# Optimization experiments

Measured on AMD Instinct MI355X. Metric: run time of the kernel, lower is better.

Reference implementation:

```python
import jax, jax.numpy as jnp
import numpy as np

N = 50000        # num nodes
E = 500000       # num edges
F_IN = 128       # in_channels
F_OUT = 128      # out_channels
C = 2            # num_channels
E_DIM = 64       # edge_dim
NEG = 0.2        # leaky_relu negative slope


def setup_inputs() -> dict:
    key = jax.random.key(0)
    ks = jax.random.split(key, 8)
    glorot = lambda k, s: jax.random.normal(k, s, jnp.float32) * (1.0 / np.float32(np.sqrt(s[-1])))
    return {
        "x": jax.random.normal(ks[0], (N, F_IN), jnp.float32),
        "edge_index": jax.random.randint(ks[1], (2, E), 0, N, dtype=jnp.int32),
        "edge_attr": jax.random.normal(ks[2], (E, E_DIM), jnp.float32),
        "W_l": glorot(ks[3], (F_OUT, F_IN)),
        "channel_bias_l": jnp.zeros((C, F_OUT), jnp.float32),
        "att_shared": glorot(ks[4], (F_OUT,)),
        "att_scale": glorot(ks[5], (C,)),
        "W_edge": glorot(ks[6], (F_OUT, E_DIM)),
        "edge_bias": jnp.zeros((F_OUT, C), jnp.float32),
    }


def reference(x, edge_index, edge_attr, W_l, channel_bias_l, att_shared, att_scale, W_edge, edge_bias):
    src, tgt = edge_index[0], edge_index[1]
    # shared projection (share_weights=True -> x_r has no channel bias)
    x_base = x @ W_l.T                                      # [N, F]
    x_l = x_base[:, :, None] + channel_bias_l.T[None]       # [N, F, C]
    x_i = x_l[tgt]                                          # [E, F, C] gather targets
    x_j = x_base[src]                                       # [E, F]    gather sources (same for all channels)
    # edge embedding expanded over channels + per-channel edge bias
    edge_emb = (edge_attr @ W_edge.T)[:, :, None] + edge_bias[None]   # [E, F, C]
    attn = jax.nn.leaky_relu(x_i + x_j[:, :, None] + edge_emb, NEG)   # [E, F, C]
    # per-channel attention logits
    logits = jnp.einsum('efc,f->ec', attn, att_shared) * att_scale[None, :]  # [E, C]
    # segment softmax over target nodes (numerically stable)
    m = jax.ops.segment_max(logits, tgt, num_segments=N)    # [N, C]
    m = jnp.where(jnp.isfinite(m), m, 0.0)
    e = jnp.exp(logits - m[tgt])
    s = jax.ops.segment_sum(e, tgt, num_segments=N)
    alpha = e / (s[tgt] + 1e-16)                            # [E, C]
    # weighted messages and scatter-add aggregation
    msgs = (x_j[:, :, None] + edge_emb) * alpha[:, None, :] # [E, F, C]
    agg = jax.ops.segment_sum(msgs, tgt, num_segments=N)    # [N, F, C]
    # concat=True: channel-major concat along feature dim -> [N, C*F]
    out = agg.transpose(0, 2, 1).reshape(N, C * F_OUT)
    return out, alpha
```

## Files before the change

### kernel.cpp

```cpp
#include <hip/hip_runtime.h>
#include <hip/hip_bf16.h>

#define NN 50000
#define NE 500000
#define F 128
#define K_IN 128
#define ED 64
#define C 2
#define NEG 0.2f
#define FLTMAX 3.402823466e38f
#define PROJ_BLOCKS 782
#define HIST_BLOCKS 1954

typedef __attribute__((ext_vector_type(8))) short short8;
typedef __attribute__((ext_vector_type(8))) unsigned short ushort8;
typedef __attribute__((ext_vector_type(4))) float f32x4;

__device__ __forceinline__ short bf16r(float f) {
    unsigned u = __float_as_uint(f);
    unsigned r = (u + 0x7fffu + ((u >> 16) & 1u)) >> 16;
    return (short)r;
}

__device__ __forceinline__ float b2f(unsigned short v) {
    return __uint_as_float(((unsigned)v) << 16);
}

__device__ __forceinline__ short8 ldfrag(const float* base) {
    const float4* p = reinterpret_cast<const float4*>(base);
    float4 v0 = p[0], v1 = p[1];
    short8 r;
    r[0] = bf16r(v0.x); r[1] = bf16r(v0.y); r[2] = bf16r(v0.z); r[3] = bf16r(v0.w);
    r[4] = bf16r(v1.x); r[5] = bf16r(v1.y); r[6] = bf16r(v1.z); r[7] = bf16r(v1.w);
    return r;
}

__device__ __forceinline__ short8 cvt8(float4 v0, float4 v1) {
    short8 r;
    r[0] = bf16r(v0.x); r[1] = bf16r(v0.y); r[2] = bf16r(v0.z); r[3] = bf16r(v0.w);
    r[4] = bf16r(v1.x); r[5] = bf16r(v1.y); r[6] = bf16r(v1.z); r[7] = bf16r(v1.w);
    return r;
}

__global__ __launch_bounds__(256) void proj_hist(const float* __restrict__ x,
                                                 const float* __restrict__ W_l,
                                                 unsigned short* __restrict__ xbp,
                                                 const int* __restrict__ ei,
                                                 int* __restrict__ counts) {
    if (blockIdx.x < PROJ_BLOCKS) {
        int lane = threadIdx.x & 63, wid = threadIdx.x >> 6;
        int grp = lane >> 4, col = lane & 15;
        int tile = blockIdx.x * 4 + wid;
        if (tile >= NN / 16) return;
        int n0 = tile * 16;

        f32x4 acc[8];
#pragma unroll
        for (int t = 0; t < 8; ++t) acc[t] = (f32x4){0.f, 0.f, 0.f, 0.f};

        const float* arow = x + (size_t)(n0 + col) * K_IN + grp * 8;
#pragma unroll
        for (int kt = 0; kt < 4; ++kt) {
            short8 a = ldfrag(arow + kt * 32);
#pragma unroll
            for (int t = 0; t < 8; ++t) {
                short8 b = ldfrag(W_l + (size_t)(t * 16 + col) * K_IN + kt * 32 + grp * 8);
                acc[t] = __builtin_amdgcn_mfma_f32_16x16x32_bf16(a, b, acc[t], 0, 0, 0);
            }
        }
#pragma unroll
        for (int j = 0; j < 4; ++j) {
            ushort8 o;
#pragma unroll
            for (int t = 0; t < 8; ++t) o[t] = (unsigned short)bf16r(acc[t][j]);
            *reinterpret_cast<ushort8*>(xbp + (size_t)(n0 + grp * 4 + j) * F + col * 8) = o;
        }
    } else {
        int e = (blockIdx.x - PROJ_BLOCKS) * 256 + threadIdx.x;
        if (e < NE) atomicAdd(&counts[ei[NE + e]], 1);
    }
}

__global__ __launch_bounds__(1024) void scan1_kernel(const int* __restrict__ counts,
                                                     int* __restrict__ offs,
                                                     int* __restrict__ bsum) {
    __shared__ int wsum[16];
    int i = blockIdx.x * 1024 + threadIdx.x;
    int lane = threadIdx.x & 63, w = threadIdx.x >> 6;
    int v = (i < NN) ? counts[i] : 0;
    int x = v;
#pragma unroll
    for (int off = 1; off < 64; off <<= 1) {
        int y = __shfl_up(x, off, 64);
        if (lane >= off) x += y;
    }
    if (lane == 63) wsum[w] = x;
    __syncthreads();
    if (w == 0 && lane < 16) {
        int t = wsum[lane];
#pragma unroll
        for (int off = 1; off < 16; off <<= 1) {
            int y = __shfl_up(t, off, 16);
            if (lane >= off) t += y;
        }
        wsum[lane] = t;
    }
    __syncthreads();
    int woff = (w == 0) ? 0 : wsum[w - 1];
    if (i < NN) offs[i] = woff + x - v;
    if (threadIdx.x == 1023) bsum[blockIdx.x] = woff + x;
}

__global__ __launch_bounds__(1024) void scan3b_kernel(int* __restrict__ offs,
                                                      const int* __restrict__ bsum,
                                                      int* __restrict__ cursor) {
    __shared__ int carry_s;
    if (threadIdx.x < 64) {
        int v = (threadIdx.x < blockIdx.x) ? bsum[threadIdx.x] : 0;
#pragma unroll
        for (int off = 32; off; off >>= 1) v += __shfl_xor(v, off, 64);
        if (threadIdx.x == 0) carry_s = v;
    }
    __syncthreads();
    int carry = carry_s;
    int i = blockIdx.x * 1024 + threadIdx.x;
    if (i < NN) {
        int o = offs[i] + carry;
        offs[i] = o;
        cursor[i] = o;
    }
    if (blockIdx.x == 0 && threadIdx.x == 0) offs[NN] = NE;
}

__global__ void scatter_kernel(const int* __restrict__ ei, int* __restrict__ cursor,
                               int2* __restrict__ perm2, int* __restrict__ tgts) {
    int e = blockIdx.x * blockDim.x + threadIdx.x;
    if (e < NE) {
        int src = ei[e];
        int tgt = ei[NE + e];
        int p = atomicAdd(&cursor[tgt], 1);
        int2 v; v.x = e; v.y = src;
        perm2[p] = v;
        tgts[p] = tgt;
    }
}

template<int MODE>
__global__ __launch_bounds__(256) void edge_logits_mfma(
    const int2* __restrict__ perm2, const int* __restrict__ tgts,
    const float* __restrict__ ea,
    const unsigned short* __restrict__ xbp, const float* __restrict__ W_e,
    const float* __restrict__ cb, const float* __restrict__ att,
    const float* __restrict__ att_sc, const float* __restrict__ ebias,
    float* __restrict__ lgs, unsigned short* __restrict__ msg) {
    int lane = threadIdx.x & 63, wid = threadIdx.x >> 6;
    int grp = lane >> 4, col = lane & 15;

    short8 B[8][2];
#pragma unroll
    for (int t = 0; t < 8; ++t)
#pragma unroll
        for (int kt = 0; kt < 2; ++kt)
            B[t][kt] = ldfrag(W_e + (size_t)(t * 16 + col) * ED + kt * 32 + grp * 8);

    float attv[8], cbe0[8], cbe1[8];
#pragma unroll
    for (int t = 0; t < 8; ++t) {
        int f = t * 16 + col;
        attv[t] = att[f];
        cbe0[t] = cb[f] + ebias[f * 2];
        cbe1[t] = cb[F + f] + ebias[f * 2 + 1];
    }
    float as0 = att_sc[0], as1 = att_sc[1];
    float2* lgs2 = reinterpret_cast<float2*>(lgs);

    const int NT = NE / 16;
    const int stride = gridDim.x * 4;
    int tile = blockIdx.x * 4 + wid;

    int2 pe = {0, 0};
    int tgtv = 0;
    float4 rc0, rc1, rc2, rc3;
    if (tile < NT) {
        pe = perm2[tile * 16 + col];
        tgtv = tgts[tile * 16 + col];
        const float* base = ea + (size_t)pe.x * ED + grp * 8;
        const float4* ap = reinterpret_cast<const float4*>(base);
        rc0 = ap[0]; rc1 = ap[1];
        const float4* ap2 = reinterpret_cast<const float4*>(base + 32);
        rc2 = ap2[0]; rc3 = ap2[1];
    }

    for (; tile < NT; tile += stride) {
        int tn = tile + stride;
        int2 pe_n = {0, 0};
        int tgt_n = 0;
        float4 rn0 = {}, rn1 = {}, rn2 = {}, rn3 = {};
        if (tn < NT) {
            pe_n = perm2[tn * 16 + col];
            tgt_n = tgts[tn * 16 + col];
            const float* base = ea + (size_t)pe_n.x * ED + grp * 8;
            const float4* ap = reinterpret_cast<const float4*>(base);
            rn0 = ap[0]; rn1 = ap[1];
            const float4* ap2 = reinterpret_cast<const float4*>(base + 32);
            rn2 = ap2[0]; rn3 = ap2[1];
        }

        int p0 = tile * 16;
        int srcv = pe.y;
        int tgti[4];
        ushort8 xsv[4];
#pragma unroll
        for (int j = 0; j < 4; ++j) {
            int idx = grp * 4 + j;
            int src = __shfl(srcv, idx, 16);
            tgti[j] = __shfl(tgtv, idx, 16);
            xsv[j] = *reinterpret_cast<const ushort8*>(
                xbp + (size_t)src * F + col * 8);
        }

        short8 a0 = cvt8(rc0, rc1);
        short8 a1 = cvt8(rc2, rc3);
        f32x4 acc[8];
#pragma unroll
        for (int t = 0; t < 8; ++t) acc[t] = (f32x4){0.f, 0.f, 0.f, 0.f};
#pragma unroll
        for (int t = 0; t < 8; ++t) {
            acc[t] = __builtin_amdgcn_mfma_f32_16x16x32_bf16(a0, B[t][0], acc[t], 0, 0, 0);
            acc[t] = __builtin_amdgcn_mfma_f32_16x16x32_bf16(a1, B[t][1], acc[t], 0, 0, 0);
        }
#pragma unroll
        for (int j = 0; j < 4; ++j) {
            int idx = grp * 4 + j;
            ushort8 xs = xsv[j];
            ushort8 xt = *reinterpret_cast<const ushort8*>(
                xbp + (size_t)tgti[j] * F + col * 8);
            float q0 = 0.f, q1 = 0.f;
            ushort8 mvs;
#pragma unroll
            for (int t = 0; t < 8; ++t) {
                float mv = b2f(xs[t]) + acc[t][j];
                mvs[t] = (unsigned short)bf16r(mv);
                float s = mv + b2f(xt[t]);
                float u0 = s + cbe0[t]; u0 = fmaxf(u0, NEG * u0);
                float u1 = s + cbe1[t]; u1 = fmaxf(u1, NEG * u1);
                q0 = fmaf(u0, attv[t], q0);
                q1 = fmaf(u1, attv[t], q1);
            }
            if (MODE >= 1)
                *reinterpret_cast<ushort8*>(msg + (size_t)(p0 + idx) * F + col * 8) = mvs;
#pragma unroll
            for (int off = 8; off; off >>= 1) {
                q0 += __shfl_xor(q0, off, 16);
                q1 += __shfl_xor(q1, off, 16);
            }
            if (col == 0) {
                float2 o; o.x = q0 * as0; o.y = q1 * as1;
                lgs2[p0 + idx] = o;
            }
        }
        pe = pe_n; tgtv = tgt_n;
        rc0 = rn0; rc1 = rn1; rc2 = rn2; rc3 = rn3;
    }
}

__global__ __launch_bounds__(512) void agg_msg(
    const int* __restrict__ offs, const int2* __restrict__ perm2,
    const unsigned short* __restrict__ msg, const float* __restrict__ ebias,
    const float* __restrict__ lgs,
    float* __restrict__ out, float* __restrict__ alpha_out) {
    int lane = threadIdx.x & 63;
    int node = blockIdx.x * 8 + (threadIdx.x >> 6);
    if (node >= NN) return;
    int beg = offs[node], end = offs[node + 1];
    int deg = end - beg;
    float* orow = out + (size_t)node * (C * F);
    float2* orow2 = reinterpret_cast<float2*>(orow);
    if (deg == 0) {
        float2 z; z.x = 0.f; z.y = 0.f;
        orow2[lane] = z; orow2[64 + lane] = z;
        return;
    }
    const float2* lgs2 = reinterpret_cast<const float2*>(lgs);
    float2* al2 = reinterpret_cast<float2*>(alpha_out);

    float m0 = -FLTMAX, m1 = -FLTMAX;
    for (int j = beg + lane; j < end; j += 64) {
        float2 lg = lgs2[j];
        m0 = fmaxf(m0, lg.x); m1 = fmaxf(m1, lg.y);
    }
#pragma unroll
    for (int off = 32; off; off >>= 1) {
        m0 = fmaxf(m0, __shfl_xor(m0, off, 64));
        m1 = fmaxf(m1, __shfl_xor(m1, off, 64));
    }
    float su0 = 0.f, su1 = 0.f;
    for (int j = beg + lane; j < end; j += 64) {
        float2 lg = lgs2[j];
        su0 += __expf(lg.x - m0); su1 += __expf(lg.y - m1);
    }
#pragma unroll
    for (int off = 32; off; off >>= 1) {
        su0 += __shfl_xor(su0, off, 64);
        su1 += __shfl_xor(su1, off, 64);
    }
    float inv0 = 1.f / (su0 + 1e-16f), inv1 = 1.f / (su1 + 1e-16f);

    float g00 = 0.f, g01 = 0.f, g10 = 0.f, g11 = 0.f;
    for (int cb0 = beg; cb0 < end; cb0 += 64) {
        int cnt = min(64, end - cb0);
        int jl = cb0 + min(lane, cnt - 1);
        bool act = lane < cnt;
        int el = perm2[jl].x;
        float2 lgl = lgs2[jl];
        float e0v = act ? __expf(lgl.x - m0) : 0.f;
        float e1v = act ? __expf(lgl.y - m1) : 0.f;
        if (act) { float2 av; av.x = e0v * inv0; av.y = e1v * inv1; al2[el] = av; }
#pragma unroll 4
        for (int i = 0; i < cnt; ++i) {
            float a0 = __shfl(e0v, i, 64) * inv0;
            float a1 = __shfl(e1v, i, 64) * inv1;
            unsigned mv = *reinterpret_cast<const unsigned*>(
                msg + (size_t)(cb0 + i) * F + lane * 2);
            float f0 = __uint_as_float((mv & 0xffffu) << 16);
            float f1 = __uint_as_float(mv & 0xffff0000u);
            g00 = fmaf(a0, f0, g00); g01 = fmaf(a0, f1, g01);
            g10 = fmaf(a1, f0, g10); g11 = fmaf(a1, f1, g11);
        }
    }
    float sa0 = su0 * inv0, sa1 = su1 * inv1;
    int q0i = 2 * lane;
    int f0i = (q0i & 7) * 16 + (q0i >> 3);
    int f1i = f0i + 16;
    orow[f0i]       = g00 + ebias[f0i * 2] * sa0;
    orow[f1i]       = g01 + ebias[f1i * 2] * sa0;
    orow[F + f0i]   = g10 + ebias[f0i * 2 + 1] * sa1;
    orow[F + f1i]   = g11 + ebias[f1i * 2 + 1] * sa1;
}

__device__ __forceinline__ float xbval(const unsigned short* __restrict__ xbp,
                                       int n, int f) {
    return b2f(xbp[(size_t)n * F + (f & 15) * 8 + (f >> 4)]);
}

__global__ __launch_bounds__(512) void agg_fast(
    const int* __restrict__ offs, const int2* __restrict__ perm2,
    const float* __restrict__ ea, const unsigned short* __restrict__ xbp,
    const float* __restrict__ ebias, const float* __restrict__ lgs,
    float* __restrict__ out, float* __restrict__ alpha_out,
    float* __restrict__ H) {
    int lane = threadIdx.x & 63;
    int node = blockIdx.x * 8 + (threadIdx.x >> 6);
    if (node >= NN) return;
    int beg = offs[node], end = offs[node + 1];
    int deg = end - beg;
    float* orow = out + (size_t)node * (C * F);
    float* hrow = H + (size_t)node * (C * ED);

    if (deg == 0) {
        orow[lane] = 0.f; orow[64 + lane] = 0.f;
        orow[128 + lane] = 0.f; orow[192 + lane] = 0.f;
        if (lane < 32) { hrow[lane * 4] = 0.f; hrow[lane * 4 + 1] = 0.f;
                         hrow[lane * 4 + 2] = 0.f; hrow[lane * 4 + 3] = 0.f; }
        return;
    }
    const float2* lgs2 = reinterpret_cast<const float2*>(lgs);
    float2* al2 = reinterpret_cast<float2*>(alpha_out);

    float m0 = -FLTMAX, m1 = -FLTMAX;
    for (int j = beg + lane; j < end; j += 64) {
        float2 lg = lgs2[j];
        m0 = fmaxf(m0, lg.x); m1 = fmaxf(m1, lg.y);
    }
#pragma unroll
    for (int off = 32; off; off >>= 1) {
        m0 = fmaxf(m0, __shfl_xor(m0, off, 64));
        m1 = fmaxf(m1, __shfl_xor(m1, off, 64));
    }
    float s0 = 0.f, s1 = 0.f;
    for (int j = beg + lane; j < end; j += 64) {
        float2 lg = lgs2[j];
        s0 += __expf(lg.x - m0); s1 += __expf(lg.y - m1);
    }
#pragma unroll
    for (int off = 32; off; off >>= 1) {
        s0 += __shfl_xor(s0, off, 64);
        s1 += __shfl_xor(s1, off, 64);
    }
    float inv0 = 1.f / (s0 + 1e-16f), inv1 = 1.f / (s1 + 1e-16f);

    float h0 = 0.f, h1 = 0.f;
    float g00 = 0.f, g01 = 0.f, g10 = 0.f, g11 = 0.f;
    for (int j = beg; j < end; ++j) {
        int2 pe; pe.x = __builtin_amdgcn_readfirstlane(perm2[j].x);
        pe.y = __builtin_amdgcn_readfirstlane(perm2[j].y);
        float2 lg = lgs2[j];
        float a0 = __builtin_amdgcn_readfirstlane(__expf(lg.x - m0)) * inv0;
        float a1 = __builtin_amdgcn_readfirstlane(__expf(lg.y - m1)) * inv1;
        if (lane == 0) { float2 av; av.x = a0; av.y = a1; al2[pe.x] = av; }
        float av = ea[(size_t)pe.x * ED + lane];
        h0 = fmaf(a0, av, h0); h1 = fmaf(a1, av, h1);
        float xv0 = xbval(xbp, pe.y, lane);
        float xv1 = xbval(xbp, pe.y, 64 + lane);
        g00 = fmaf(a0, xv0, g00); g01 = fmaf(a1, xv0, g01);
        g10 = fmaf(a0, xv1, g10); g11 = fmaf(a1, xv1, g11);
    }
    hrow[lane] = h0; hrow[64 + lane] = h1;
    float sa0 = s0 * inv0, sa1 = s1 * inv1;
    orow[lane]       = g00 + ebias[lane * 2] * sa0;
    orow[64 + lane]  = g10 + ebias[(64 + lane) * 2] * sa0;
    orow[128 + lane] = g01 + ebias[lane * 2 + 1] * sa1;
    orow[192 + lane] = g11 + ebias[(64 + lane) * 2 + 1] * sa1;
}

__global__ __launch_bounds__(512) void emb_gemm(const float* __restrict__ H,
                                                const float* __restrict__ W_e,
                                                float* __restrict__ out) {
    __shared__ float WeT[ED][F];
    for (int i = threadIdx.x; i < ED * F; i += 512) {
        int f = i & (F - 1), k = i >> 7;
        WeT[k][f] = W_e[(size_t)f * ED + k];
    }
    __syncthreads();
    int lane = threadIdx.x & 63, wid = threadIdx.x >> 6;
    const int R = NN * C;
    for (int row = blockIdx.x * 8 + wid; row < R; row += gridDim.x * 8) {
        float h = H[(size_t)row * ED + lane];
        float m0 = 0.f, m1 = 0.f;
#pragma unroll
        for (int k = 0; k < ED; ++k) {
            float hk = __shfl(h, k, 64);
            m0 = fmaf(hk, WeT[k][lane], m0);
            m1 = fmaf(hk, WeT[k][lane + 64], m1);
        }
        float* op = out + (size_t)row * F;
        op[lane] += m0;
        op[lane + 64] += m1;
    }
}

extern "C" void kernel_launch(void* const* d_in, const int* in_sizes, int n_in,
                              void* d_out, int out_size, void* d_ws, size_t ws_size,
                              hipStream_t stream) {
    const float* x      = (const float*)d_in[0];
    const int*   ei     = (const int*)d_in[1];
    const float* ea     = (const float*)d_in[2];
    const float* W_l    = (const float*)d_in[3];
    const float* cb     = (const float*)d_in[4];
    const float* att    = (const float*)d_in[5];
    const float* att_sc = (const float*)d_in[6];
    const float* W_e    = (const float*)d_in[7];
    const float* ebias  = (const float*)d_in[8];

    float* out = (float*)d_out;
    float* alpha_out = out + (size_t)NN * C * F;

    float* ws = (float*)d_ws;
    unsigned short* xbp = (unsigned short*)ws;
    float* lgs  = ws + 6400000;
    int* ibase  = (int*)(ws + 7400000);
    int* counts = ibase;
    int* offs   = ibase + NN;
    int* bsum   = ibase + 100064;
    int* tgts   = ibase + 100128;
    int2* perm2 = (int2*)(ibase + 100128 + NE);
    char* tail = (char*)(ibase + 100128 + 3 * NE);
    tail = (char*)(((size_t)tail + 15) & ~(size_t)15);
    size_t head_bytes = (size_t)(tail - (char*)d_ws);
    size_t msg_bytes = (size_t)NE * F * 2;
    bool use_msg = ws_size >= head_bytes + msg_bytes + 64;
    unsigned short* msg = (unsigned short*)tail;
    float* H = (float*)tail;

    hipMemsetAsync(counts, 0, NN * sizeof(int), stream);

    proj_hist<<<PROJ_BLOCKS + HIST_BLOCKS, 256, 0, stream>>>(x, W_l, xbp, ei, counts);

    const int NB = (NN + 1023) / 1024;
    scan1_kernel<<<NB, 1024, 0, stream>>>(counts, offs, bsum);
    scan3b_kernel<<<NB, 1024, 0, stream>>>(offs, bsum, counts);
    scatter_kernel<<<(NE + 255) / 256, 256, 0, stream>>>(ei, counts, perm2, tgts);

    if (use_msg) {
        edge_logits_mfma<1><<<2048, 256, 0, stream>>>(perm2, tgts, ea, xbp, W_e,
                                                      cb, att, att_sc, ebias,
                                                      lgs, msg);
        agg_msg<<<(NN + 7) / 8, 512, 0, stream>>>(offs, perm2, msg, ebias, lgs,
                                                  out, alpha_out);
    } else {
        edge_logits_mfma<0><<<2048, 256, 0, stream>>>(perm2, tgts, ea, xbp, W_e,
                                                      cb, att, att_sc, ebias,
                                                      lgs, (unsigned short*)0);
        agg_fast<<<(NN + 7) / 8, 512, 0, stream>>>(offs, perm2, ea, xbp, ebias, lgs,
                                                   out, alpha_out, H);
        emb_gemm<<<1024, 512, 0, stream>>>(H, W_e, out);
    }
}
```

Before: 252.5 us.

## Stage edge-weight fragments in LDS and deepen gather prefetch in edge logits kernel

Moves the W_edge bf16 MFMA B-fragments from per-thread registers into shared memory to free registers. The index loads (perm2/tgts) are prefetched two tiles ahead instead of one, and the target-row gather is hoisted next to the source-row gather so both are in flight before the MFMAs. This aims to hide the latency of the dependent gathers and may raise occupancy. In exchange it adds LDS reads inside the hot loop, a block barrier at startup, and extra live registers for the deeper prefetch.

```diff
diff --git a/kernel.cpp b/kernel.cpp
--- a/kernel.cpp
+++ b/kernel.cpp
@@ -153,15 +153,15 @@
     const float* __restrict__ cb, const float* __restrict__ att,
     const float* __restrict__ att_sc, const float* __restrict__ ebias,
     float* __restrict__ lgs, unsigned short* __restrict__ msg) {
+    __shared__ short8 Blds[16][64];
     int lane = threadIdx.x & 63, wid = threadIdx.x >> 6;
     int grp = lane >> 4, col = lane & 15;
 
-    short8 B[8][2];
-#pragma unroll
-    for (int t = 0; t < 8; ++t)
-#pragma unroll
-        for (int kt = 0; kt < 2; ++kt)
-            B[t][kt] = ldfrag(W_e + (size_t)(t * 16 + col) * ED + kt * 32 + grp * 8);
+    for (int fidx = threadIdx.x; fidx < 1024; fidx += 256) {
+        int l = fidx & 63, kt = (fidx >> 6) & 1, t = fidx >> 7;
+        int g2 = l >> 4, c2 = l & 15;
+        Blds[t * 2 + kt][l] = ldfrag(W_e + (size_t)(t * 16 + c2) * ED + kt * 32 + g2 * 8);
+    }
 
     float attv[8], cbe0[8], cbe1[8];
 #pragma unroll
@@ -173,17 +173,27 @@
     }
     float as0 = att_sc[0], as1 = att_sc[1];
     float2* lgs2 = reinterpret_cast<float2*>(lgs);
+    __syncthreads();
 
     const int NT = NE / 16;
     const int stride = gridDim.x * 4;
     int tile = blockIdx.x * 4 + wid;
 
-    int2 pe = {0, 0};
-    int tgtv = 0;
+    int2 pe = {0, 0}, pe_n = {0, 0};
+    int tgtv = 0, tgt_n = 0;
     float4 rc0, rc1, rc2, rc3;
     if (tile < NT) {
         pe = perm2[tile * 16 + col];
         tgtv = tgts[tile * 16 + col];
+    }
+    {
+        int tb = tile + stride;
+        if (tb < NT) {
+            pe_n = perm2[tb * 16 + col];
+            tgt_n = tgts[tb * 16 + col];
+        }
+    }
+    if (tile < NT) {
         const float* base = ea + (size_t)pe.x * ED + grp * 8;
         const float4* ap = reinterpret_cast<const float4*>(base);
         rc0 = ap[0]; rc1 = ap[1];
@@ -193,23 +203,12 @@
 
     for (; tile < NT; tile += stride) {
         int tn = tile + stride;
-        int2 pe_n = {0, 0};
-        int tgt_n = 0;
-        float4 rn0 = {}, rn1 = {}, rn2 = {}, rn3 = {};
-        if (tn < NT) {
-            pe_n = perm2[tn * 16 + col];
-            tgt_n = tgts[tn * 16 + col];
-            const float* base = ea + (size_t)pe_n.x * ED + grp * 8;
-            const float4* ap = reinterpret_cast<const float4*>(base);
-            rn0 = ap[0]; rn1 = ap[1];
-            const float4* ap2 = reinterpret_cast<const float4*>(base + 32);
-            rn2 = ap2[0]; rn3 = ap2[1];
-        }
-
+        int tnn = tile + 2 * stride;
         int p0 = tile * 16;
         int srcv = pe.y;
+
         int tgti[4];
-        ushort8 xsv[4];
+        ushort8 xsv[4], xtv[4];
 #pragma unroll
         for (int j = 0; j < 4; ++j) {
             int idx = grp * 4 + j;
@@ -217,6 +216,22 @@
             tgti[j] = __shfl(tgtv, idx, 16);
             xsv[j] = *reinterpret_cast<const ushort8*>(
                 xbp + (size_t)src * F + col * 8);
+            xtv[j] = *reinterpret_cast<const ushort8*>(
+                xbp + (size_t)tgti[j] * F + col * 8);
+        }
+        float4 rn0 = {}, rn1 = {}, rn2 = {}, rn3 = {};
+        if (tn < NT) {
+            const float* base = ea + (size_t)pe_n.x * ED + grp * 8;
+            const float4* ap = reinterpret_cast<const float4*>(base);
+            rn0 = ap[0]; rn1 = ap[1];
+            const float4* ap2 = reinterpret_cast<const float4*>(base + 32);
+            rn2 = ap2[0]; rn3 = ap2[1];
+        }
+        int2 pe_nn = {0, 0};
+        int tgt_nn = 0;
+        if (tnn < NT) {
+            pe_nn = perm2[tnn * 16 + col];
+            tgt_nn = tgts[tnn * 16 + col];
         }
 
         short8 a0 = cvt8(rc0, rc1);
@@ -226,15 +241,14 @@
         for (int t = 0; t < 8; ++t) acc[t] = (f32x4){0.f, 0.f, 0.f, 0.f};
 #pragma unroll
         for (int t = 0; t < 8; ++t) {
-            acc[t] = __builtin_amdgcn_mfma_f32_16x16x32_bf16(a0, B[t][0], acc[t], 0, 0, 0);
-            acc[t] = __builtin_amdgcn_mfma_f32_16x16x32_bf16(a1, B[t][1], acc[t], 0, 0, 0);
+            acc[t] = __builtin_amdgcn_mfma_f32_16x16x32_bf16(a0, Blds[t * 2][lane], acc[t], 0, 0, 0);
+            acc[t] = __builtin_amdgcn_mfma_f32_16x16x32_bf16(a1, Blds[t * 2 + 1][lane], acc[t], 0, 0, 0);
         }
 #pragma unroll
         for (int j = 0; j < 4; ++j) {
             int idx = grp * 4 + j;
             ushort8 xs = xsv[j];
-            ushort8 xt = *reinterpret_cast<const ushort8*>(
-                xbp + (size_t)tgti[j] * F + col * 8);
+            ushort8 xt = xtv[j];
             float q0 = 0.f, q1 = 0.f;
             ushort8 mvs;
 #pragma unroll
@@ -260,6 +274,7 @@
             }
         }
         pe = pe_n; tgtv = tgt_n;
+        pe_n = pe_nn; tgt_n = tgt_nn;
         rc0 = rn0; rc1 = rn1; rc2 = rn2; rc3 = rn3;
     }
 }
```

New measurement: 221.1 us, median of 2. 1.14x faster.
